# Optimization experiments

Hardware: AMD Instinct MI355X
Metric: run time of the kernel (lower is better)

Reference implementation:

```python
import jax, jax.numpy as jnp
import numpy as np

B, CIN, C, N, K = 2, 64, 128, 8192, 16
GROUPS = C // 16
EPS = 1e-5


def lrelu(x):
    return jnp.where(x >= 0, x, 0.1 * x)


def conv1d(x, w, b):  # x:(B,Ci,N) w:(Co,Ci)
    return jnp.einsum('oc,bcn->bon', w, x) + b[None, :, None]


def conv2d(x, w, b):  # x:(B,Ci,N,K) w:(Co,Ci)
    return jnp.einsum('oc,bcnk->bonk', w, x) + b[None, :, None, None]


def groupnorm(x, gamma, beta, groups=GROUPS):
    # normalize over (C/groups, *spatial) per sample per group
    b, c = x.shape[0], x.shape[1]
    xr = x.reshape(b, groups, -1)
    mean = xr.mean(-1, keepdims=True)
    var = xr.var(-1, keepdims=True)
    xn = ((xr - mean) * jax.lax.rsqrt(var + EPS)).reshape(x.shape)
    shp = (1, c) + (1,) * (x.ndim - 2)
    return xn * gamma.reshape(shp) + beta.reshape(shp)


def knn_idx(xyz, k):  # xyz:(B,3,N) -> idx:(B,N,K)
    pts = jnp.transpose(xyz, (0, 2, 1))  # (B,N,3)
    sq = jnp.sum(pts * pts, axis=-1)  # (B,N)
    inner = jnp.einsum('bnc,bmc->bnm', pts, pts)
    d2 = sq[:, :, None] + sq[:, None, :] - 2.0 * inner  # (B,N,N)
    _, idx = jax.lax.top_k(-d2, k)
    return idx


def group(x, idx):  # x:(B,C,N) idx:(B,N,K) -> (B,C,N,K)
    b, c, n = x.shape
    k = idx.shape[-1]
    idxe = jnp.broadcast_to(idx.reshape(b, 1, n * k), (b, c, n * k))
    return jnp.take_along_axis(x, idxe, axis=2).reshape(b, c, n, k)


def reference(xyz, feat, pre_w, pre_b, wq_w, wq_b, wk_w, wk_b, wv_w, wv_b,
              pos1_w, pos1_b, pos1_g, pos1_be, pos2_w, pos2_b,
              att1_w, att1_b, att1_g, att1_be, att2_w, att2_b,
              post_w, post_b, post_g, post_be):
    idx = knn_idx(xyz, K)  # (B,N,K)
    new_feat = conv1d(feat, pre_w, pre_b)  # (B,C,N)
    rel = group(xyz, idx) - xyz[:, :, :, None]  # (B,3,N,K)
    pos = lrelu(groupnorm(conv2d(rel, pos1_w, pos1_b), pos1_g, pos1_be))
    pos = conv2d(pos, pos2_w, pos2_b)  # (B,C,N,K)
    q = conv1d(new_feat, wq_w, wq_b)
    k = group(conv1d(new_feat, wk_w, wk_b), idx)  # (B,C,N,K)
    v = group(conv1d(new_feat, wv_w, wv_b), idx)
    att = q[:, :, :, None] - k + pos
    att = lrelu(groupnorm(conv2d(att, att1_w, att1_b), att1_g, att1_be))
    att = conv2d(att, att2_w, att2_b)
    att = jax.nn.softmax(att, axis=3)
    out = jnp.sum(att * v, axis=3)  # (B,C,N)
    out = lrelu(groupnorm(conv1d(out + new_feat, post_w, post_b), post_g, post_be))
    return out


def setup_inputs():
    key = jax.random.key(0)
    ks = jax.random.split(key, 16)
    s = 0.05
    d = {
        'xyz': jax.random.normal(ks[0], (B, 3, N), jnp.float32),
        'feat': jax.random.normal(ks[1], (B, CIN, N), jnp.float32),
        'pre_w': jax.random.normal(ks[2], (C, CIN), jnp.float32) * s,
        'pre_b': jnp.zeros((C,), jnp.float32),
        'wq_w': jax.random.normal(ks[3], (C, C), jnp.float32) * s,
        'wq_b': jnp.zeros((C,), jnp.float32),
        'wk_w': jax.random.normal(ks[4], (C, C), jnp.float32) * s,
        'wk_b': jnp.zeros((C,), jnp.float32),
        'wv_w': jax.random.normal(ks[5], (C, C), jnp.float32) * s,
        'wv_b': jnp.zeros((C,), jnp.float32),
        'pos1_w': jax.random.normal(ks[6], (C, 3), jnp.float32) * s,
        'pos1_b': jnp.zeros((C,), jnp.float32),
        'pos1_g': jnp.ones((C,), jnp.float32),
        'pos1_be': jnp.zeros((C,), jnp.float32),
        'pos2_w': jax.random.normal(ks[7], (C, C), jnp.float32) * s,
        'pos2_b': jnp.zeros((C,), jnp.float32),
        'att1_w': jax.random.normal(ks[8], (C, C), jnp.float32) * s,
        'att1_b': jnp.zeros((C,), jnp.float32),
        'att1_g': jnp.ones((C,), jnp.float32),
        'att1_be': jnp.zeros((C,), jnp.float32),
        'att2_w': jax.random.normal(ks[9], (C, C), jnp.float32) * s,
        'att2_b': jnp.zeros((C,), jnp.float32),
        'post_w': jax.random.normal(ks[10], (C, C), jnp.float32) * s,
        'post_b': jnp.zeros((C,), jnp.float32),
        'post_g': jnp.ones((C,), jnp.float32),
        'post_be': jnp.zeros((C,), jnp.float32),
    }
    return d
```

## Files before the change

### kernel.cpp

```cpp
#include <hip/hip_runtime.h>
#include <hip/hip_bf16.h>

#define BB 2
#define NN 8192
#define CC 128
#define CIN_ 64
#define KK 16
#define EPSV 1e-5f

typedef __attribute__((ext_vector_type(8))) short short8;
typedef __attribute__((ext_vector_type(4))) float f32x4;

static const size_t OFF_NF   = 262144;
static const size_t OFF_OUT2 = OFF_NF  + 2097152;
static const size_t OFF_Y    = OFF_OUT2 + 2097152;
static const size_t OFF_AQB  = OFF_Y   + 16777216;
static const size_t OFF_AKB  = OFF_AQB + 1048576;
static const size_t OFF_VFB  = OFF_AKB + 1048576;
static const size_t OFF_WQ2  = OFF_VFB + 1048576;
static const size_t OFF_WK2  = OFF_WQ2 + 16384;
static const size_t OFF_PWT  = OFF_WK2 + 16384;
static const size_t OFF_W2B  = OFF_PWT + 16384;
static const size_t OFF_A2B  = OFF_W2B + 8192;
static const size_t OFF_BY   = OFF_A2B + 8192;
static const size_t OFF_RST  = OFF_BY  + 128;
static const size_t OFF_REDA = OFF_RST + 32;
static const size_t OFF_REDP = OFF_REDA + 32;
static const size_t OFF_S1   = OFF_REDP + 32;
static const size_t OFF_T1   = OFF_S1 + 256;
static const size_t OFF_S2   = OFF_T1 + 256;
static const size_t OFF_T2   = OFF_S2 + 256;
static const size_t OFF_S3   = OFF_T2 + 256;
static const size_t OFF_T3   = OFF_S3 + 256;
static const size_t OFF_PTS4 = OFF_T3 + 256;
static const size_t OFF_PTA  = OFF_PTS4 + 65536;
static const size_t OFF_PTP  = OFF_PTA + 65536;

__device__ __forceinline__ unsigned fkey_u(float d) {
  unsigned u = __float_as_uint(d);
  return (u & 0x80000000u) ? ~u : (u | 0x80000000u);
}
__device__ __forceinline__ unsigned long long shflx64(unsigned long long v, int m) {
  int lo = __shfl_xor((int)(unsigned)(v & 0xffffffffu), m, 64);
  int hi = __shfl_xor((int)(unsigned)(v >> 32), m, 64);
  return ((unsigned long long)(unsigned)hi << 32) | (unsigned)lo;
}
__device__ __forceinline__ float bf2f(unsigned short u) {
  return __uint_as_float((unsigned)u << 16);
}
__device__ __forceinline__ unsigned short f2bf(float f) {
  __hip_bfloat16 h = __float2bfloat16(f);
  unsigned short r;
  __builtin_memcpy(&r, &h, 2);
  return r;
}
__device__ __forceinline__ unsigned pack2bf(float a, float b) {
  return (unsigned)f2bf(a) | ((unsigned)f2bf(b) << 16);
}

__global__ __launch_bounds__(128) void prep_weights(
    const float* __restrict__ att1_w, const float* __restrict__ wq_w, const float* __restrict__ wk_w,
    const float* __restrict__ pos2_w, const float* __restrict__ att2_w, const float* __restrict__ post_w,
    const float* __restrict__ wq_b, const float* __restrict__ wk_b, const float* __restrict__ pos2_b,
    const float* __restrict__ att1_b,
    float* __restrict__ WQ2, float* __restrict__ WK2, __hip_bfloat16* __restrict__ W2b,
    __hip_bfloat16* __restrict__ A2b, float* __restrict__ PWT, float* __restrict__ bias_y) {
  int blk = blockIdx.x, t = threadIdx.x;
  if (blk < 128) {
    int c = blk;
    __shared__ float row[128];
    row[t] = att1_w[c * 128 + t];
    __syncthreads();
    float sq = 0.f, sk = 0.f, sp = 0.f;
    for (int m = 0; m < 128; ++m) {
      float r = row[m];
      sq = fmaf(r, wq_w[m * 128 + t], sq);
      sk = fmaf(r, wk_w[m * 128 + t], sk);
      sp = fmaf(r, pos2_w[m * 128 + t], sp);
    }
    WQ2[c * 128 + t] = sq;
    WK2[c * 128 + t] = sk;
    W2b[c * 128 + t] = __float2bfloat16(sp);
  } else if (blk == 128) {
    for (int e = t; e < 16384; e += 128) {
      int c = e >> 7, cp = e & 127;
      A2b[e] = __float2bfloat16(att2_w[e]);
      PWT[cp * 128 + c] = post_w[e];
    }
  } else {
    float s = att1_b[t];
    for (int m = 0; m < 128; ++m)
      s = fmaf(att1_w[t * 128 + m], wq_b[m] - wk_b[m] + pos2_b[m], s);
    bias_y[t] = s;
  }
}

__global__ __launch_bounds__(256) void pts4_kernel(const float* __restrict__ xyz,
                                                   float4* __restrict__ pts4) {
  int e = blockIdx.x * 256 + threadIdx.x;
  int b = e >> 13, n = e & 8191;
  const float* X = xyz + b * 3 * NN;
  float x = X[n], y = X[NN + n], z = X[2 * NN + n];
  pts4[e] = make_float4(-2.0f * x, -2.0f * y, -2.0f * z, fmaf(z, z, fmaf(y, y, x * x)));
}

#define SLOTS 96
__global__ __launch_bounds__(512) void knn_kernel(const float4* __restrict__ pts4,
                                                  int* __restrict__ idxb) {
  __shared__ float4 tile[2048];
  __shared__ unsigned long long list[32][SLOTS];
  __shared__ float chm[32][33];
  __shared__ int cnt[32];
  int t = threadIdx.x;
  int wid = t >> 6, lane = t & 63;
  int q = lane & 31, sub = lane >> 5;
  int blk = blockIdx.x;
  int b = blk >> 8;
  int q0 = (blk & 255) << 5;
  const float4* P = pts4 + b * NN;
  float4 qv = P[q0 + q];
  float qx = -0.5f * qv.x, qy = -0.5f * qv.y, qz = -0.5f * qv.z;
  if (t < 32) cnt[t] = 0;
  int tbase = (wid << 8) + (sub << 7);

  {
    float4 r0 = P[t], r1 = P[512 + t], r2 = P[1024 + t], r3 = P[1536 + t];
    tile[t] = r0; tile[512 + t] = r1; tile[1024 + t] = r2; tile[1536 + t] = r3;
  }
  __syncthreads();
  for (int s = 0; s < 4; ++s) {
    float4 p0, p1, p2, p3;
    if (s < 3) {
      const float4* S = P + ((s + 1) << 11);
      p0 = S[t]; p1 = S[512 + t]; p2 = S[1024 + t]; p3 = S[1536 + t];
    }
    const float4* T = &tile[tbase];
    float mm = 3.4e38f;
    for (int i = 0; i < 128; i += 8) {
      float d[8];
#pragma unroll
      for (int u = 0; u < 8; ++u) {
        float4 cv = T[i + u];
        d[u] = fmaf(qx, cv.x, fmaf(qy, cv.y, fmaf(qz, cv.z, cv.w)));
      }
      mm = fminf(mm, fminf(fminf(fminf(d[0], d[1]), fminf(d[2], d[3])),
                           fminf(fminf(d[4], d[5]), fminf(d[6], d[7]))));
    }
    mm = fminf(mm, __shfl_xor(mm, 32));
    __syncthreads();
    if (s < 3) {
      tile[t] = p0; tile[512 + t] = p1; tile[1024 + t] = p2; tile[1536 + t] = p3;
    }
    if (lane < 32) chm[lane][(s << 3) + wid] = mm;
    __syncthreads();
  }

  float tau;
  {
    float v[32];
#pragma unroll
    for (int i = 0; i < 32; ++i) v[i] = chm[q][i];
    float lo = v[0], hi = v[0];
#pragma unroll
    for (int i = 1; i < 32; ++i) { lo = fminf(lo, v[i]); hi = fmaxf(hi, v[i]); }
    for (int it = 0; it < 12; ++it) {
      float mid = 0.5f * (lo + hi);
      int c = 0;
#pragma unroll
      for (int i = 0; i < 32; ++i) c += (v[i] <= mid) ? 1 : 0;
      if (c >= 16) hi = mid; else lo = mid;
    }
    tau = hi;
  }

  {
    float4 r0 = P[t], r1 = P[512 + t], r2 = P[1024 + t], r3 = P[1536 + t];
    __syncthreads();
    tile[t] = r0; tile[512 + t] = r1; tile[1024 + t] = r2; tile[1536 + t] = r3;
  }
  __syncthreads();
  for (int s = 0; s < 4; ++s) {
    float4 p0, p1, p2, p3;
    if (s < 3) {
      const float4* S = P + ((s + 1) << 11);
      p0 = S[t]; p1 = S[512 + t]; p2 = S[1024 + t]; p3 = S[1536 + t];
    }
    const float4* T = &tile[tbase];
    int gbase = (s << 11) + tbase;
    for (int i = 0; i < 128; i += 4) {
      float d[4];
#pragma unroll
      for (int u = 0; u < 4; ++u) {
        float4 cv = T[i + u];
        d[u] = fmaf(qx, cv.x, fmaf(qy, cv.y, fmaf(qz, cv.z, cv.w)));
      }
#pragma unroll
      for (int u = 0; u < 4; ++u) {
        if (d[u] <= tau) {
          int sl = atomicAdd(&cnt[q], 1);
          if (sl < SLOTS)
            list[q][sl] = ((unsigned long long)fkey_u(d[u]) << 32) | (unsigned)(gbase + i + u);
        }
      }
    }
    __syncthreads();
    if (s < 3) {
      tile[t] = p0; tile[512 + t] = p1; tile[1024 + t] = p2; tile[1536 + t] = p3;
    }
    __syncthreads();
  }

  for (int pp = 0; pp < 2; ++pp) {
    int qa = (wid << 2) + pp * 2, qb2 = qa + 1;
    int ca = cnt[qa]; if (ca > SLOTS) ca = SLOTS;
    int cb3 = cnt[qb2]; if (cb3 > SLOTS) cb3 = SLOTS;
    unsigned long long k0a = (lane < ca) ? list[qa][lane] : ~0ULL;
    unsigned long long k1a = (lane + 64 < ca) ? list[qa][lane + 64] : ~0ULL;
    unsigned long long k0b = (lane < cb3) ? list[qb2][lane] : ~0ULL;
    unsigned long long k1b = (lane + 64 < cb3) ? list[qb2][lane + 64] : ~0ULL;
    for (int r = 0; r < 16; ++r) {
      unsigned long long wa = (k0a < k1a) ? k0a : k1a;
      unsigned long long wb = (k0b < k1b) ? k0b : k1b;
      for (int off = 32; off; off >>= 1) {
        unsigned long long oa = shflx64(wa, off);
        unsigned long long ob = shflx64(wb, off);
        if (oa < wa) wa = oa;
        if (ob < wb) wb = ob;
      }
      if (k0a == wa) k0a = ~0ULL; else if (k1a == wa) k1a = ~0ULL;
      if (k0b == wb) k0b = ~0ULL; else if (k1b == wb) k1b = ~0ULL;
      if (lane == 0) {
        idxb[((size_t)(b * NN) + q0 + qa) * 16 + r] = (int)(wa & 0xffffffffu);
        idxb[((size_t)(b * NN) + q0 + qb2) * 16 + r] = (int)(wb & 0xffffffffu);
      }
    }
  }
}

__global__ __launch_bounds__(256) void relstats_kernel(const float* __restrict__ xyz,
                                                       const int* __restrict__ idxb,
                                                       float* __restrict__ rst) {
  int b = blockIdx.x >> 8;
  int nbase = (blockIdx.x & 255) << 5;
  const float* X = xyz + b * 3 * NN;
  float a[9];
#pragma unroll
  for (int m = 0; m < 9; ++m) a[m] = 0.f;
  for (int e = threadIdx.x; e < 512; e += 256) {
    int nn = nbase + (e >> 4);
    int kk = e & 15;
    int j = idxb[(b * NN + nn) * 16 + kk];
    float rx = X[j] - X[nn];
    float ry = X[NN + j] - X[NN + nn];
    float rz = X[2 * NN + j] - X[2 * NN + nn];
    a[0] += rx; a[1] += ry; a[2] += rz;
    a[3] = fmaf(rx, rx, a[3]); a[4] = fmaf(rx, ry, a[4]); a[5] = fmaf(rx, rz, a[5]);
    a[6] = fmaf(ry, ry, a[6]); a[7] = fmaf(ry, rz, a[7]); a[8] = fmaf(rz, rz, a[8]);
  }
  __shared__ float red[4][9];
  int lane = threadIdx.x & 63, wid = threadIdx.x >> 6;
#pragma unroll
  for (int m = 0; m < 9; ++m) {
    float v = a[m];
    for (int off = 32; off; off >>= 1) v += __shfl_xor(v, off, 64);
    if (lane == 0) red[wid][m] = v;
  }
  __syncthreads();
  if (threadIdx.x < 9) {
    float v = red[0][threadIdx.x] + red[1][threadIdx.x] + red[2][threadIdx.x] + red[3][threadIdx.x];
    atomicAdd(&rst[b * 16 + threadIdx.x], v);
  }
}

__global__ __launch_bounds__(256) void t1_kernel(const float* __restrict__ rst,
    const float* __restrict__ pos1_w, const float* __restrict__ pos1_b,
    const float* __restrict__ pos1_g, const float* __restrict__ pos1_be,
    float* __restrict__ s1, float* __restrict__ t1) {
  __shared__ float gsum[16], gsum2[16];
  int t = threadIdx.x;
  if (t < 16) { gsum[t] = 0.f; gsum2[t] = 0.f; }
  __syncthreads();
  int b = t >> 7, c = t & 127;
  const float* S = rst + b * 16;
  const float Minv = 1.0f / (float)(NN * KK);
  float mx = S[0] * Minv, my = S[1] * Minv, mz = S[2] * Minv;
  float Mxx = S[3] * Minv, Mxy = S[4] * Minv, Mxz = S[5] * Minv;
  float Myy = S[6] * Minv, Myz = S[7] * Minv, Mzz = S[8] * Minv;
  float w0 = pos1_w[c * 3], w1 = pos1_w[c * 3 + 1], w2 = pos1_w[c * 3 + 2];
  float bb = pos1_b[c];
  float wm = w0 * mx + w1 * my + w2 * mz;
  float Ey = wm + bb;
  float q = w0 * w0 * Mxx + w1 * w1 * Myy + w2 * w2 * Mzz
          + 2.f * (w0 * w1 * Mxy + w0 * w2 * Mxz + w1 * w2 * Myz);
  float Ey2 = q + 2.f * bb * wm + bb * bb;
  int g = c >> 4;
  atomicAdd(&gsum[b * 8 + g], Ey);
  atomicAdd(&gsum2[b * 8 + g], Ey2);
  __syncthreads();
  float mean = gsum[b * 8 + g] * (1.f / 16.f);
  float var = fmaxf(gsum2[b * 8 + g] * (1.f / 16.f) - mean * mean, 0.f);
  float r = rsqrtf(var + EPSV);
  float sv = pos1_g[c] * r;
  s1[t] = sv;
  t1[t] = fmaf(sv, bb, pos1_be[c] - mean * sv);
}

__global__ __launch_bounds__(256) void feat_kernel(
    const float* __restrict__ feat, const float* __restrict__ pre_w, const float* __restrict__ pre_b,
    const float* __restrict__ WQ2, const float* __restrict__ WK2,
    const float* __restrict__ wv_w, const float* __restrict__ wv_b,
    float* __restrict__ nf, __hip_bfloat16* __restrict__ AqTb,
    __hip_bfloat16* __restrict__ AkTb, __hip_bfloat16* __restrict__ vfTb) {
  int b = blockIdx.x >> 9;
  int n0 = (blockIdx.x & 511) << 4;
  __shared__ float fe[64][20];
  __shared__ float nfs[128][20];
  int t = threadIdx.x;
  for (int e = t; e < 1024; e += 256) {
    int ci = e >> 4, nn2 = e & 15;
    fe[ci][nn2] = feat[(b * 64 + ci) * NN + n0 + nn2];
  }
  __syncthreads();
  int nq = t & 3, cw = t >> 2;
  {
    float acc[2][4];
#pragma unroll
    for (int m = 0; m < 2; ++m) {
      float bv = pre_b[cw + 64 * m];
      acc[m][0] = bv; acc[m][1] = bv; acc[m][2] = bv; acc[m][3] = bv;
    }
    for (int i = 0; i < 64; ++i) {
      float4 x = *(const float4*)&fe[i][nq << 2];
      float w0 = pre_w[cw * 64 + i];
      float w1 = pre_w[(cw + 64) * 64 + i];
      acc[0][0] = fmaf(w0, x.x, acc[0][0]); acc[0][1] = fmaf(w0, x.y, acc[0][1]);
      acc[0][2] = fmaf(w0, x.z, acc[0][2]); acc[0][3] = fmaf(w0, x.w, acc[0][3]);
      acc[1][0] = fmaf(w1, x.x, acc[1][0]); acc[1][1] = fmaf(w1, x.y, acc[1][1]);
      acc[1][2] = fmaf(w1, x.z, acc[1][2]); acc[1][3] = fmaf(w1, x.w, acc[1][3]);
    }
#pragma unroll
    for (int m = 0; m < 2; ++m) {
      int c = cw + 64 * m;
      float4 v = make_float4(acc[m][0], acc[m][1], acc[m][2], acc[m][3]);
      *(float4*)&nfs[c][nq << 2] = v;
      *(float4*)&nf[(b * 128 + c) * NN + n0 + (nq << 2)] = v;
    }
  }
  __syncthreads();
  for (int s = 0; s < 3; ++s) {
    const float* Wm = (s == 0) ? WQ2 : ((s == 1) ? WK2 : wv_w);
    __hip_bfloat16* D = (s == 0) ? AqTb : ((s == 1) ? AkTb : vfTb);
    float acc[2][4];
#pragma unroll
    for (int m = 0; m < 2; ++m) {
      float bv = (s == 2) ? wv_b[cw + 64 * m] : 0.f;
      acc[m][0] = bv; acc[m][1] = bv; acc[m][2] = bv; acc[m][3] = bv;
    }
    for (int i = 0; i < 128; ++i) {
      float4 x = *(const float4*)&nfs[i][nq << 2];
      float w0 = Wm[cw * 128 + i];
      float w1 = Wm[(cw + 64) * 128 + i];
      acc[0][0] = fmaf(w0, x.x, acc[0][0]); acc[0][1] = fmaf(w0, x.y, acc[0][1]);
      acc[0][2] = fmaf(w0, x.z, acc[0][2]); acc[0][3] = fmaf(w0, x.w, acc[0][3]);
      acc[1][0] = fmaf(w1, x.x, acc[1][0]); acc[1][1] = fmaf(w1, x.y, acc[1][1]);
      acc[1][2] = fmaf(w1, x.z, acc[1][2]); acc[1][3] = fmaf(w1, x.w, acc[1][3]);
    }
#pragma unroll
    for (int m = 0; m < 2; ++m) {
      int c = cw + 64 * m;
#pragma unroll
      for (int v = 0; v < 4; ++v)
        D[(size_t)(b * NN + n0 + (nq << 2) + v) * 128 + c] = __float2bfloat16(acc[m][v]);
    }
  }
}

__global__ __launch_bounds__(256) void y_kernel_mfma(const float* __restrict__ xyz,
    const int* __restrict__ idxb, const __hip_bfloat16* __restrict__ AqTb,
    const __hip_bfloat16* __restrict__ AkTb, const __hip_bfloat16* __restrict__ W2b,
    const float* __restrict__ bias_y, const float* __restrict__ pos1_w,
    const float* __restrict__ s1, const float* __restrict__ t1,
    __hip_bfloat16* __restrict__ ybuf, float* __restrict__ partA) {
  int b = blockIdx.x >> 11;
  int pb = (blockIdx.x & 2047) * 4;
  __shared__ __align__(16) __hip_bfloat16 z_s[64][136];
  __shared__ __align__(16) __hip_bfloat16 ak_s[64][136];
  __shared__ __align__(16) float aq_s[4][128];
  __shared__ float rel_s[64][4];
  __shared__ int jj[64];
  __shared__ float gns[8], gns2[8];
  int t = threadIdx.x;
  int lane = t & 63, wid = t >> 6;
  int l15 = lane & 15, quad = lane >> 4;
  if (t < 8) { gns[t] = 0.f; gns2[t] = 0.f; }
  if (t < 64) {
    int n = pb + (t >> 4);
    int j = idxb[(b * NN + pb) * 16 + t];
    jj[t] = j;
    const float* X = xyz + b * 3 * NN;
    rel_s[t][0] = X[j] - X[n];
    rel_s[t][1] = X[NN + j] - X[NN + n];
    rel_s[t][2] = X[2 * NN + j] - X[2 * NN + n];
  }
  for (int e = t; e < 512; e += 256) {
    int pt = e >> 7, c = e & 127;
    aq_s[pt][c] = bf2f(((const unsigned short*)AqTb)[((size_t)(b * NN) + pb + pt) * 128 + c]) + bias_y[c];
  }
  __syncthreads();
  {
    int cpp = t & 63, pg = t >> 6;
    int cp0 = cpp * 2;
    float w00 = pos1_w[cp0 * 3], w01 = pos1_w[cp0 * 3 + 1], w02 = pos1_w[cp0 * 3 + 2];
    float w10 = pos1_w[cp0 * 3 + 3], w11 = pos1_w[cp0 * 3 + 4], w12 = pos1_w[cp0 * 3 + 5];
    float sa = s1[b * 128 + cp0], ta = t1[b * 128 + cp0];
    float sb = s1[b * 128 + cp0 + 1], tb = t1[b * 128 + cp0 + 1];
#pragma unroll
    for (int i = 0; i < 16; ++i) {
      int pix = pg * 16 + i;
      float rx = rel_s[pix][0], ry = rel_s[pix][1], rz = rel_s[pix][2];
      float u0 = fmaf(w02, rz, fmaf(w01, ry, w00 * rx));
      float u1 = fmaf(w12, rz, fmaf(w11, ry, w10 * rx));
      float z0 = fmaf(sa, u0, ta); z0 = (z0 >= 0.f) ? z0 : 0.1f * z0;
      float z1 = fmaf(sb, u1, tb); z1 = (z1 >= 0.f) ? z1 : 0.1f * z1;
      *(unsigned*)&z_s[pix][cp0] = pack2bf(z0, z1);
    }
  }
  for (int e = t; e < 4096; e += 256) {
    int pix = e >> 6, cpp = e & 63;
    *(unsigned*)&ak_s[pix][cpp * 2] =
        *(const unsigned*)((const unsigned short*)AkTb + ((size_t)(b * NN) + jj[pix]) * 128 + cpp * 2);
  }
  short8 afr[2][4];
#pragma unroll
  for (int m2 = 0; m2 < 2; ++m2) {
    int row = (wid * 2 + m2) * 16 + l15;
#pragma unroll
    for (int k0 = 0; k0 < 4; ++k0)
      afr[m2][k0] = *(const short8*)((const unsigned short*)W2b + row * 128 + k0 * 32 + quad * 8);
  }
  __syncthreads();
  f32x4 acc[2][4];
#pragma unroll
  for (int m2 = 0; m2 < 2; ++m2)
#pragma unroll
    for (int nt = 0; nt < 4; ++nt) acc[m2][nt] = (f32x4){0.f, 0.f, 0.f, 0.f};
#pragma unroll
  for (int k0 = 0; k0 < 4; ++k0) {
#pragma unroll
    for (int nt = 0; nt < 4; ++nt) {
      short8 bfr = *(const short8*)&z_s[nt * 16 + l15][k0 * 32 + quad * 8];
      acc[0][nt] = __builtin_amdgcn_mfma_f32_16x16x32_bf16(afr[0][k0], bfr, acc[0][nt], 0, 0, 0);
      acc[1][nt] = __builtin_amdgcn_mfma_f32_16x16x32_bf16(afr[1][k0], bfr, acc[1][nt], 0, 0, 0);
    }
  }
  float lsum[2] = {0.f, 0.f}, lsum2[2] = {0.f, 0.f};
#pragma unroll
  for (int m2 = 0; m2 < 2; ++m2) {
    int c0 = (wid * 2 + m2) * 16 + quad * 4;
#pragma unroll
    for (int nt = 0; nt < 4; ++nt) {
      int pix = nt * 16 + l15;
      ushort4 au = *(ushort4*)&ak_s[pix][c0];
      float4 aq = *(float4*)&aq_s[nt][c0];
      f32x4 a = acc[m2][nt];
      float v0 = a[0] + aq.x - bf2f(au.x);
      float v1 = a[1] + aq.y - bf2f(au.y);
      float v2 = a[2] + aq.z - bf2f(au.z);
      float v3 = a[3] + aq.w - bf2f(au.w);
      lsum[m2] += (v0 + v1) + (v2 + v3);
      lsum2[m2] += fmaf(v0, v0, fmaf(v1, v1, fmaf(v2, v2, v3 * v3)));
      ushort4 yo;
      yo.x = f2bf(v0); yo.y = f2bf(v1); yo.z = f2bf(v2); yo.w = f2bf(v3);
      *(ushort4*)&ak_s[pix][c0] = yo;
    }
  }
#pragma unroll
  for (int m2 = 0; m2 < 2; ++m2) {
    float s = lsum[m2], s2 = lsum2[m2];
    for (int msk = 1; msk < 64; msk <<= 1) {
      s += __shfl_xor(s, msk);
      s2 += __shfl_xor(s2, msk);
    }
    if (lane == 0) {
      atomicAdd(&gns[wid * 2 + m2], s);
      atomicAdd(&gns2[wid * 2 + m2], s2);
    }
  }
  __syncthreads();
  size_t ybase = ((size_t)(b * NN) + pb) * 16;
  unsigned short* yb = (unsigned short*)ybuf;
  for (int e = t; e < 4096; e += 256) {
    int pix = e >> 6, cpp = e & 63;
    *(unsigned*)(yb + (ybase + pix) * 128 + cpp * 2) = *(unsigned*)&ak_s[pix][cpp * 2];
  }
  if (t < 8) {
    partA[(size_t)t * 4096 + blockIdx.x] = gns[t];
    partA[(size_t)(8 + t) * 4096 + blockIdx.x] = gns2[t];
  }
}

__global__ __launch_bounds__(256) void gnred_kernel(const float* __restrict__ part,
                                                    float* __restrict__ red) {
  int k = blockIdx.x;
  int pb = k >> 4, idx = k & 15;
  const float* p = part + (size_t)idx * 4096 + pb * 2048;
  float s = 0.f;
  for (int i = threadIdx.x; i < 2048; i += 256) s += p[i];
  __shared__ float rs[4];
  int lane = threadIdx.x & 63, wid = threadIdx.x >> 6;
  for (int off = 32; off; off >>= 1) s += __shfl_xor(s, off);
  if (lane == 0) rs[wid] = s;
  __syncthreads();
  if (threadIdx.x == 0) red[k] = rs[0] + rs[1] + rs[2] + rs[3];
}

__global__ __launch_bounds__(256) void gnaff_kernel(const float* __restrict__ red,
    const float* __restrict__ gamma, const float* __restrict__ beta, float Minv,
    float* __restrict__ sarr, float* __restrict__ tarr) {
  int t = threadIdx.x;
  int b = t >> 7, c = t & 127, g = c >> 4;
  float S = red[b * 16 + g], S2 = red[b * 16 + 8 + g];
  float mean = S * Minv;
  float var = fmaxf(S2 * Minv - mean * mean, 0.f);
  float r = rsqrtf(var + EPSV);
  float sv = gamma[c] * r;
  sarr[t] = sv;
  tarr[t] = beta[c] - mean * sv;
}

__global__ __launch_bounds__(256) void att_out_kernel(const __hip_bfloat16* __restrict__ ybuf,
    const int* __restrict__ idxb, const float* __restrict__ s2, const float* __restrict__ t2,
    const __hip_bfloat16* __restrict__ A2b, const __hip_bfloat16* __restrict__ vfTb,
    const float* __restrict__ nf, const float* __restrict__ PWT, const float* __restrict__ post_b,
    float* __restrict__ out2, float* __restrict__ partP) {
  int b = blockIdx.x >> 11;
  int pb = (blockIdx.x & 2047) * 4;
  __shared__ __align__(16) union HS {
    unsigned short h[64][136];
    float sc[2][128][17];
  } hs;
  __shared__ __align__(16) __hip_bfloat16 v_s[64][136];
  __shared__ __align__(16) float opre[4][132];
  __shared__ int jj[64];
  __shared__ float gns[8], gns2[8];
  int t = threadIdx.x;
  int lane = t & 63, wid = t >> 6;
  int l15 = lane & 15, quad = lane >> 4;
  if (t < 8) { gns[t] = 0.f; gns2[t] = 0.f; }
  if (t < 64) jj[t] = idxb[(b * NN + pb) * 16 + t];
  __syncthreads();
  size_t ybase = ((size_t)(b * NN) + pb) * 16;
  const unsigned short* yb = (const unsigned short*)ybuf;
  {
    int cpp = t & 63, pg = t >> 6;
    int c0 = cpp * 2;
    float sa = s2[b * 128 + c0], ta = t2[b * 128 + c0];
    float sb = s2[b * 128 + c0 + 1], tb = t2[b * 128 + c0 + 1];
#pragma unroll
    for (int i = 0; i < 16; ++i) {
      int pix = pg * 16 + i;
      unsigned u = *(const unsigned*)(yb + (ybase + pix) * 128 + c0);
      float y0 = bf2f((unsigned short)(u & 0xffff));
      float y1 = bf2f((unsigned short)(u >> 16));
      float h0 = fmaf(sa, y0, ta); h0 = (h0 >= 0.f) ? h0 : 0.1f * h0;
      float h1 = fmaf(sb, y1, tb); h1 = (h1 >= 0.f) ? h1 : 0.1f * h1;
      *(unsigned*)&hs.h[pix][c0] = pack2bf(h0, h1);
    }
  }
  for (int e = t; e < 4096; e += 256) {
    int pix = e >> 6, cpp = e & 63;
    *(unsigned*)&v_s[pix][cpp * 2] =
        *(const unsigned*)((const unsigned short*)vfTb + ((size_t)(b * NN) + jj[pix]) * 128 + cpp * 2);
  }
  short8 afr[2][4];
#pragma unroll
  for (int m2 = 0; m2 < 2; ++m2) {
    int row = (wid * 2 + m2) * 16 + l15;
#pragma unroll
    for (int k0 = 0; k0 < 4; ++k0)
      afr[m2][k0] = *(const short8*)((const unsigned short*)A2b + row * 128 + k0 * 32 + quad * 8);
  }
  __syncthreads();
  f32x4 acc[2][4];
#pragma unroll
  for (int m2 = 0; m2 < 2; ++m2)
#pragma unroll
    for (int nt = 0; nt < 4; ++nt) acc[m2][nt] = (f32x4){0.f, 0.f, 0.f, 0.f};
#pragma unroll
  for (int k0 = 0; k0 < 4; ++k0) {
#pragma unroll
    for (int nt = 0; nt < 4; ++nt) {
      short8 bfr = *(const short8*)&hs.h[nt * 16 + l15][k0 * 32 + quad * 8];
      acc[0][nt] = __builtin_amdgcn_mfma_f32_16x16x32_bf16(afr[0][k0], bfr, acc[0][nt], 0, 0, 0);
      acc[1][nt] = __builtin_amdgcn_mfma_f32_16x16x32_bf16(afr[1][k0], bfr, acc[1][nt], 0, 0, 0);
    }
  }
  int pidx = t >> 7;
  int cch = t & 127;
#pragma unroll
  for (int pass = 0; pass < 2; ++pass) {
    __syncthreads();
#pragma unroll
    for (int ntl = 0; ntl < 2; ++ntl) {
      int nt = pass * 2 + ntl;
#pragma unroll
      for (int m2 = 0; m2 < 2; ++m2) {
        int cb = (wid * 2 + m2) * 16 + quad * 4;
        f32x4 a = acc[m2][nt];
#pragma unroll
        for (int r = 0; r < 4; ++r) hs.sc[ntl][cb + r][l15] = a[r];
      }
    }
    __syncthreads();
    {
      int p = pass * 2 + pidx;
      float nfv = nf[(size_t)(b * 128 + cch) * NN + pb + p];
      const float* srow = hs.sc[pidx][cch];
      float sv[16];
#pragma unroll
      for (int k = 0; k < 16; ++k) sv[k] = srow[k];
      float mx = sv[0];
#pragma unroll
      for (int k = 1; k < 16; ++k) mx = fmaxf(mx, sv[k]);
      float sm = 0.f, dot = 0.f;
#pragma unroll
      for (int k = 0; k < 16; ++k) {
        float e = __expf(sv[k] - mx);
        sm += e;
        float vv = bf2f(*(const unsigned short*)&v_s[p * 16 + k][cch]);
        dot = fmaf(e, vv, dot);
      }
      opre[p][cch] = dot / sm + nfv;
    }
  }
  __syncthreads();
  {
    int c = t & 127, g = t >> 7;
    float a0 = post_b[c], a1 = a0;
    for (int cp = 0; cp < 128; ++cp) {
      float w = PWT[cp * 128 + c];
      a0 = fmaf(w, opre[g * 2][cp], a0);
      a1 = fmaf(w, opre[g * 2 + 1][cp], a1);
    }
    out2[(size_t)(b * 128 + c) * NN + pb + g * 2] = a0;
    out2[(size_t)(b * 128 + c) * NN + pb + g * 2 + 1] = a1;
    atomicAdd(&gns[c >> 4], a0 + a1);
    atomicAdd(&gns2[c >> 4], fmaf(a0, a0, a1 * a1));
  }
  __syncthreads();
  if (t < 8) {
    partP[(size_t)t * 4096 + blockIdx.x] = gns[t];
    partP[(size_t)(8 + t) * 4096 + blockIdx.x] = gns2[t];
  }
}

__global__ __launch_bounds__(256) void final_kernel(const float* __restrict__ out2,
    const float* __restrict__ s3, const float* __restrict__ t3, float* __restrict__ out) {
  int e = blockIdx.x * 256 + threadIdx.x;
  int c = (e >> 13) & 127, b = e >> 20;
  float v = fmaf(s3[b * 128 + c], out2[e], t3[b * 128 + c]);
  out[e] = (v >= 0.f) ? v : 0.1f * v;
}

extern "C" void kernel_launch(void* const* d_in, const int* in_sizes, int n_in,
                              void* d_out, int out_size, void* d_ws, size_t ws_size,
                              hipStream_t stream) {
  (void)in_sizes; (void)n_in; (void)out_size; (void)ws_size;
  const float* xyz     = (const float*)d_in[0];
  const float* feat    = (const float*)d_in[1];
  const float* pre_w   = (const float*)d_in[2];
  const float* pre_b   = (const float*)d_in[3];
  const float* wq_w    = (const float*)d_in[4];
  const float* wq_b    = (const float*)d_in[5];
  const float* wk_w    = (const float*)d_in[6];
  const float* wk_b    = (const float*)d_in[7];
  const float* wv_w    = (const float*)d_in[8];
  const float* wv_b    = (const float*)d_in[9];
  const float* pos1_w  = (const float*)d_in[10];
  const float* pos1_b  = (const float*)d_in[11];
  const float* pos1_g  = (const float*)d_in[12];
  const float* pos1_be = (const float*)d_in[13];
  const float* pos2_w  = (const float*)d_in[14];
  const float* pos2_b  = (const float*)d_in[15];
  const float* att1_w  = (const float*)d_in[16];
  const float* att1_b  = (const float*)d_in[17];
  const float* att1_g  = (const float*)d_in[18];
  const float* att1_be = (const float*)d_in[19];
  const float* att2_w  = (const float*)d_in[20];
  const float* post_w  = (const float*)d_in[22];
  const float* post_b  = (const float*)d_in[23];
  const float* post_g  = (const float*)d_in[24];
  const float* post_be = (const float*)d_in[25];

  float* W = (float*)d_ws;
  int* idxb = (int*)d_ws;
  float* nf   = W + OFF_NF;
  float* out2 = W + OFF_OUT2;
  __hip_bfloat16* ybuf = (__hip_bfloat16*)(W + OFF_Y);
  __hip_bfloat16* AqTb = (__hip_bfloat16*)(W + OFF_AQB);
  __hip_bfloat16* AkTb = (__hip_bfloat16*)(W + OFF_AKB);
  __hip_bfloat16* vfTb = (__hip_bfloat16*)(W + OFF_VFB);
  float* WQ2  = W + OFF_WQ2;
  float* WK2  = W + OFF_WK2;
  float* PWT  = W + OFF_PWT;
  __hip_bfloat16* W2b = (__hip_bfloat16*)(W + OFF_W2B);
  __hip_bfloat16* A2b = (__hip_bfloat16*)(W + OFF_A2B);
  float* BY   = W + OFF_BY;
  float* RST  = W + OFF_RST;
  float* REDA = W + OFF_REDA;
  float* REDP = W + OFF_REDP;
  float* S1 = W + OFF_S1; float* T1 = W + OFF_T1;
  float* S2 = W + OFF_S2; float* T2 = W + OFF_T2;
  float* S3 = W + OFF_S3; float* T3 = W + OFF_T3;
  float4* PTS4 = (float4*)(W + OFF_PTS4);
  float* PARTA = W + OFF_PTA;
  float* PARTP = W + OFF_PTP;

  hipMemsetAsync(RST, 0, 32 * sizeof(float), stream);

  prep_weights<<<130, 128, 0, stream>>>(att1_w, wq_w, wk_w, pos2_w, att2_w, post_w,
                                        wq_b, wk_b, pos2_b, att1_b,
                                        WQ2, WK2, W2b, A2b, PWT, BY);
  pts4_kernel<<<64, 256, 0, stream>>>(xyz, PTS4);
  knn_kernel<<<512, 512, 0, stream>>>(PTS4, idxb);
  relstats_kernel<<<512, 256, 0, stream>>>(xyz, idxb, RST);
  t1_kernel<<<1, 256, 0, stream>>>(RST, pos1_w, pos1_b, pos1_g, pos1_be, S1, T1);
  feat_kernel<<<1024, 256, 0, stream>>>(feat, pre_w, pre_b, WQ2, WK2, wv_w, wv_b,
                                        nf, AqTb, AkTb, vfTb);
  y_kernel_mfma<<<4096, 256, 0, stream>>>(xyz, idxb, AqTb, AkTb, W2b, BY, pos1_w, S1, T1, ybuf, PARTA);
  gnred_kernel<<<32, 256, 0, stream>>>(PARTA, REDA);
  gnaff_kernel<<<1, 256, 0, stream>>>(REDA, att1_g, att1_be, 1.0f / 2097152.0f, S2, T2);
  att_out_kernel<<<4096, 256, 0, stream>>>(ybuf, idxb, S2, T2, A2b, vfTb, nf, PWT, post_b, out2, PARTP);
  gnred_kernel<<<32, 256, 0, stream>>>(PARTP, REDP);
  gnaff_kernel<<<1, 256, 0, stream>>>(REDP, post_g, post_be, 1.0f / 131072.0f, S3, T3);
  final_kernel<<<8192, 256, 0, stream>>>(out2, S3, T3, (float*)d_out);
}
```

Before: 389.7 us.

## Restructure kNN to keep query points in registers and stream candidates

The kNN kernel now handles 16 queries per 256-thread block instead of 32 queries per 512-thread block. Each lane keeps all 16 queries in registers and reads candidate points straight from global memory, so the shared-memory candidate tile and its double-buffered staging and barriers are gone. Per-chunk minima for the threshold estimate are reduced with wave shuffles, and thresholds are shared through LDS before the filtering pass. This raises per-thread register use and arithmetic intensity and adds shuffle reductions and more divergent LDS atomics per lane, in exchange for removing LDS traffic and synchronisation.

```diff
diff --git a/kernel.cpp b/kernel.cpp
--- a/kernel.cpp
+++ b/kernel.cpp
@@ -105,61 +105,60 @@
 }
 
 #define SLOTS 96
-__global__ __launch_bounds__(512) void knn_kernel(const float4* __restrict__ pts4,
+__global__ __launch_bounds__(256) void knn_kernel(const float4* __restrict__ pts4,
                                                   int* __restrict__ idxb) {
-  __shared__ float4 tile[2048];
-  __shared__ unsigned long long list[32][SLOTS];
-  __shared__ float chm[32][33];
-  __shared__ int cnt[32];
+  __shared__ unsigned long long list[16][SLOTS];
+  __shared__ float chm[16][33];
+  __shared__ float taus[16];
+  __shared__ int cnt[16];
   int t = threadIdx.x;
   int wid = t >> 6, lane = t & 63;
-  int q = lane & 31, sub = lane >> 5;
   int blk = blockIdx.x;
-  int b = blk >> 8;
-  int q0 = (blk & 255) << 5;
+  int b = blk >> 9;
+  int q0 = (blk & 511) << 4;
   const float4* P = pts4 + b * NN;
-  float4 qv = P[q0 + q];
-  float qx = -0.5f * qv.x, qy = -0.5f * qv.y, qz = -0.5f * qv.z;
-  if (t < 32) cnt[t] = 0;
-  int tbase = (wid << 8) + (sub << 7);
-
-  {
-    float4 r0 = P[t], r1 = P[512 + t], r2 = P[1024 + t], r3 = P[1536 + t];
-    tile[t] = r0; tile[512 + t] = r1; tile[1024 + t] = r2; tile[1536 + t] = r3;
-  }
-  __syncthreads();
-  for (int s = 0; s < 4; ++s) {
-    float4 p0, p1, p2, p3;
-    if (s < 3) {
-      const float4* S = P + ((s + 1) << 11);
-      p0 = S[t]; p1 = S[512 + t]; p2 = S[1024 + t]; p3 = S[1536 + t];
-    }
-    const float4* T = &tile[tbase];
-    float mm = 3.4e38f;
-    for (int i = 0; i < 128; i += 8) {
-      float d[8];
-#pragma unroll
-      for (int u = 0; u < 8; ++u) {
-        float4 cv = T[i + u];
-        d[u] = fmaf(qx, cv.x, fmaf(qy, cv.y, fmaf(qz, cv.z, cv.w)));
-      }
-      mm = fminf(mm, fminf(fminf(fminf(d[0], d[1]), fminf(d[2], d[3])),
-                           fminf(fminf(d[4], d[5]), fminf(d[6], d[7]))));
-    }
-    mm = fminf(mm, __shfl_xor(mm, 32));
-    __syncthreads();
-    if (s < 3) {
-      tile[t] = p0; tile[512 + t] = p1; tile[1024 + t] = p2; tile[1536 + t] = p3;
-    }
-    if (lane < 32) chm[lane][(s << 3) + wid] = mm;
-    __syncthreads();
-  }
-
-  float tau;
-  {
+  if (t < 16) cnt[t] = 0;
+  float qsx[16], qsy[16], qsz[16];
+#pragma unroll
+  for (int j = 0; j < 16; ++j) {
+    float4 qv = P[q0 + j];
+    qsx[j] = qv.x; qsy[j] = qv.y; qsz[j] = qv.z;
+  }
+
+  for (int ch = 0; ch < 8; ++ch) {
+    const float4* Pc = P + (wid << 11) + (ch << 8);
+    float4 cv0 = Pc[lane];
+    float4 cv1 = Pc[64 + lane];
+    float4 cv2 = Pc[128 + lane];
+    float4 cv3 = Pc[192 + lane];
+    float c0x = -0.5f * cv0.x, c0y = -0.5f * cv0.y, c0z = -0.5f * cv0.z;
+    float c1x = -0.5f * cv1.x, c1y = -0.5f * cv1.y, c1z = -0.5f * cv1.z;
+    float c2x = -0.5f * cv2.x, c2y = -0.5f * cv2.y, c2z = -0.5f * cv2.z;
+    float c3x = -0.5f * cv3.x, c3y = -0.5f * cv3.y, c3z = -0.5f * cv3.z;
+    float mn[16];
+#pragma unroll
+    for (int j = 0; j < 16; ++j) {
+      float d0 = fmaf(qsx[j], c0x, fmaf(qsy[j], c0y, fmaf(qsz[j], c0z, cv0.w)));
+      float d1 = fmaf(qsx[j], c1x, fmaf(qsy[j], c1y, fmaf(qsz[j], c1z, cv1.w)));
+      float d2 = fmaf(qsx[j], c2x, fmaf(qsy[j], c2y, fmaf(qsz[j], c2z, cv2.w)));
+      float d3 = fmaf(qsx[j], c3x, fmaf(qsy[j], c3y, fmaf(qsz[j], c3z, cv3.w)));
+      mn[j] = fminf(fminf(d0, d1), fminf(d2, d3));
+    }
+#pragma unroll
+    for (int off = 32; off; off >>= 1)
+#pragma unroll
+      for (int j = 0; j < 16; ++j) mn[j] = fminf(mn[j], __shfl_xor(mn[j], off));
+    if (lane == 0) {
+#pragma unroll
+      for (int j = 0; j < 16; ++j) chm[j][(wid << 3) + ch] = mn[j];
+    }
+  }
+  __syncthreads();
+
+  if (t < 16) {
     float v[32];
 #pragma unroll
-    for (int i = 0; i < 32; ++i) v[i] = chm[q][i];
+    for (int i = 0; i < 32; ++i) v[i] = chm[t][i];
     float lo = v[0], hi = v[0];
 #pragma unroll
     for (int i = 1; i < 32; ++i) { lo = fminf(lo, v[i]); hi = fmaxf(hi, v[i]); }
@@ -170,45 +169,28 @@
       for (int i = 0; i < 32; ++i) c += (v[i] <= mid) ? 1 : 0;
       if (c >= 16) hi = mid; else lo = mid;
     }
-    tau = hi;
-  }
-
-  {
-    float4 r0 = P[t], r1 = P[512 + t], r2 = P[1024 + t], r3 = P[1536 + t];
-    __syncthreads();
-    tile[t] = r0; tile[512 + t] = r1; tile[1024 + t] = r2; tile[1536 + t] = r3;
-  }
-  __syncthreads();
-  for (int s = 0; s < 4; ++s) {
-    float4 p0, p1, p2, p3;
-    if (s < 3) {
-      const float4* S = P + ((s + 1) << 11);
-      p0 = S[t]; p1 = S[512 + t]; p2 = S[1024 + t]; p3 = S[1536 + t];
-    }
-    const float4* T = &tile[tbase];
-    int gbase = (s << 11) + tbase;
-    for (int i = 0; i < 128; i += 4) {
-      float d[4];
-#pragma unroll
-      for (int u = 0; u < 4; ++u) {
-        float4 cv = T[i + u];
-        d[u] = fmaf(qx, cv.x, fmaf(qy, cv.y, fmaf(qz, cv.z, cv.w)));
+    taus[t] = hi;
+  }
+  __syncthreads();
+  float tauv[16];
+#pragma unroll
+  for (int j = 0; j < 16; ++j) tauv[j] = taus[j];
+
+  for (int i = 0; i < 32; ++i) {
+    int ci = (wid << 11) + (i << 6) + lane;
+    float4 cv = P[ci];
+    float cx = -0.5f * cv.x, cy = -0.5f * cv.y, cz = -0.5f * cv.z;
+#pragma unroll
+    for (int j = 0; j < 16; ++j) {
+      float d = fmaf(qsx[j], cx, fmaf(qsy[j], cy, fmaf(qsz[j], cz, cv.w)));
+      if (d <= tauv[j]) {
+        int sl = atomicAdd(&cnt[j], 1);
+        if (sl < SLOTS)
+          list[j][sl] = ((unsigned long long)fkey_u(d) << 32) | (unsigned)ci;
       }
-#pragma unroll
-      for (int u = 0; u < 4; ++u) {
-        if (d[u] <= tau) {
-          int sl = atomicAdd(&cnt[q], 1);
-          if (sl < SLOTS)
-            list[q][sl] = ((unsigned long long)fkey_u(d[u]) << 32) | (unsigned)(gbase + i + u);
-        }
-      }
-    }
-    __syncthreads();
-    if (s < 3) {
-      tile[t] = p0; tile[512 + t] = p1; tile[1024 + t] = p2; tile[1536 + t] = p3;
-    }
-    __syncthreads();
-  }
+    }
+  }
+  __syncthreads();
 
   for (int pp = 0; pp < 2; ++pp) {
     int qa = (wid << 2) + pp * 2, qb2 = qa + 1;
@@ -722,7 +704,7 @@
                                         wq_b, wk_b, pos2_b, att1_b,
                                         WQ2, WK2, W2b, A2b, PWT, BY);
   pts4_kernel<<<64, 256, 0, stream>>>(xyz, PTS4);
-  knn_kernel<<<512, 512, 0, stream>>>(PTS4, idxb);
+  knn_kernel<<<1024, 256, 0, stream>>>(PTS4, idxb);
   relstats_kernel<<<512, 256, 0, stream>>>(xyz, idxb, RST);
   t1_kernel<<<1, 256, 0, stream>>>(RST, pos1_w, pos1_b, pos1_g, pos1_be, S1, T1);
   feat_kernel<<<1024, 256, 0, stream>>>(feat, pre_w, pre_b, WQ2, WK2, wv_w, wv_b,
```

Measured after the change: 402.1 us. 3.2% more time.
